# Kernel tuning notes

Hardware: AMD Instinct MI355X
Metric: run time of the kernel (lower is better)

The kernel has to match this reference:

```python
import jax, jax.numpy as jnp
import numpy as np
import math


def _get_slopes(n):
    def pow2(n):
        start = 2 ** (-2 ** (-(math.log2(n) - 3)))
        return [start * start ** i for i in range(n)]
    if math.log2(n).is_integer():
        return pow2(n)
    c = 2 ** math.floor(math.log2(n))
    return pow2(c) + _get_slopes(2 * c)[0::2][: n - c]


NUM_HEADS = 16


def setup_inputs() -> dict:
    slopes = jnp.asarray(np.array(_get_slopes(NUM_HEADS), dtype=np.float32))
    return {"slopes": slopes, "seq_len": 2048, "batch_size": 4}


def reference(slopes, seq_len, batch_size):
    # relative position |i - j|: (S, S)
    pos = jnp.arange(seq_len)
    rel = jnp.abs(pos[:, None] - pos[None, :]).astype(slopes.dtype)
    # (H, S, S): -slope_h * |i - j|
    bias = -slopes[:, None, None] * rel[None, :, :]
    # torch .repeat(batch_size, 1, 1) -> (B*H, S, S)
    return jnp.tile(bias, (batch_size, 1, 1))
```

## Files before the change

### kernel.cpp

```cpp
#include <hip/hip_runtime.h>

#define NUM_HEADS 16u

__global__ __launch_bounds__(256) void alibi_bias_kernel(
    const float* __restrict__ slopes,
    const int* __restrict__ seq_p,
    float* __restrict__ out,
    unsigned int n_total)
{
    const unsigned int S  = (unsigned int)seq_p[0];
    const unsigned int S4 = S >> 2;
    const unsigned int n4 = n_total >> 2;
    const unsigned int stride = gridDim.x * blockDim.x;
    float4* __restrict__ out4 = (float4*)out;

    for (unsigned int v = blockIdx.x * blockDim.x + threadIdx.x; v < n4; v += stride) {
        unsigned int jv  = v % S4;
        unsigned int row = v / S4;
        unsigned int i   = row % S;
        unsigned int h   = (row / S) % NUM_HEADS;

        float nslope = -slopes[h];
        int   ii = (int)i;
        int   j0 = (int)(jv << 2);

        float4 o;
        o.x = nslope * (float)abs(ii - j0);
        o.y = nslope * (float)abs(ii - (j0 + 1));
        o.z = nslope * (float)abs(ii - (j0 + 2));
        o.w = nslope * (float)abs(ii - (j0 + 3));
        out4[v] = o;
    }

    for (unsigned int e = (n4 << 2) + blockIdx.x * blockDim.x + threadIdx.x;
         e < n_total; e += stride) {
        unsigned int j   = e % S;
        unsigned int row = e / S;
        unsigned int i   = row % S;
        unsigned int h   = (row / S) % NUM_HEADS;
        out[e] = -slopes[h] * (float)abs((int)i - (int)j);
    }
}

extern "C" void kernel_launch(void* const* d_in, const int* in_sizes, int n_in,
                              void* d_out, int out_size, void* d_ws, size_t ws_size,
                              hipStream_t stream) {
    const float* slopes = (const float*)d_in[0];
    const int*   seq_p  = (const int*)d_in[1];
    float*       out    = (float*)d_out;

    unsigned int n  = (unsigned int)out_size;
    unsigned int n4 = n >> 2;

    const int block = 256;
    unsigned int blocks_needed = (n4 + block - 1) / block;
    unsigned int grid = blocks_needed < 2048u ? blocks_needed : 2048u;
    if (grid < 1u) grid = 1u;

    alibi_bias_kernel<<<dim3(grid), dim3(block), 0, stream>>>(slopes, seq_p, out, n);
}
```

Measured before the change: 203.9 us.

## Process row-aligned chunks per block with nontemporal vector stores

Each block now handles whole 2048-element chunks that lie inside a single row, so the row, head and slope are worked out once per chunk rather than per float4 with divisions. Each thread writes two float4s using nontemporal stores, which avoids polluting the cache on this write-only output. The grid grows to up to 16384 blocks. The fast path needs S to be a multiple of 2048; any other length falls back to a scalar loop.

```diff
diff --git a/kernel.cpp b/kernel.cpp
--- a/kernel.cpp
+++ b/kernel.cpp
@@ -1,6 +1,9 @@
 #include <hip/hip_runtime.h>
 
 #define NUM_HEADS 16u
+#define CHUNK 2048u
+
+typedef float f32x4 __attribute__((ext_vector_type(4)));
 
 __global__ __launch_bounds__(256) void alibi_bias_kernel(
     const float* __restrict__ slopes,
@@ -8,31 +11,42 @@
     float* __restrict__ out,
     unsigned int n_total)
 {
-    const unsigned int S  = (unsigned int)seq_p[0];
-    const unsigned int S4 = S >> 2;
-    const unsigned int n4 = n_total >> 2;
-    const unsigned int stride = gridDim.x * blockDim.x;
-    float4* __restrict__ out4 = (float4*)out;
+    const unsigned int S = (unsigned int)seq_p[0];
 
-    for (unsigned int v = blockIdx.x * blockDim.x + threadIdx.x; v < n4; v += stride) {
-        unsigned int jv  = v % S4;
-        unsigned int row = v / S4;
-        unsigned int i   = row % S;
-        unsigned int h   = (row / S) % NUM_HEADS;
+    if ((S % CHUNK) == 0u) {
+        const unsigned int nchunks = n_total / CHUNK;
+        for (unsigned int c = blockIdx.x; c < nchunks; c += gridDim.x) {
+            const unsigned int base = c * CHUNK;
+            const unsigned int row  = base / S;
+            const unsigned int jst  = base - row * S;
+            const unsigned int i    = row % S;
+            const unsigned int h    = (row / S) % NUM_HEADS;
+            const float nslope = -slopes[h];
 
-        float nslope = -slopes[h];
-        int   ii = (int)i;
-        int   j0 = (int)(jv << 2);
+            const int j0 = (int)(jst + (threadIdx.x << 2));
+            float d0 = (float)((int)i - j0);
+            f32x4* __restrict__ o4 =
+                (f32x4*)(out + base) + threadIdx.x;
 
-        float4 o;
-        o.x = nslope * (float)abs(ii - j0);
-        o.y = nslope * (float)abs(ii - (j0 + 1));
-        o.z = nslope * (float)abs(ii - (j0 + 2));
-        o.w = nslope * (float)abs(ii - (j0 + 3));
-        out4[v] = o;
+            f32x4 o;
+            o.x = nslope * fabsf(d0);
+            o.y = nslope * fabsf(d0 - 1.0f);
+            o.z = nslope * fabsf(d0 - 2.0f);
+            o.w = nslope * fabsf(d0 - 3.0f);
+            __builtin_nontemporal_store(o, o4);
+
+            const float d1 = d0 - 1024.0f;
+            o.x = nslope * fabsf(d1);
+            o.y = nslope * fabsf(d1 - 1.0f);
+            o.z = nslope * fabsf(d1 - 2.0f);
+            o.w = nslope * fabsf(d1 - 3.0f);
+            __builtin_nontemporal_store(o, o4 + 256);
+        }
+        return;
     }
 
-    for (unsigned int e = (n4 << 2) + blockIdx.x * blockDim.x + threadIdx.x;
+    const unsigned int stride = gridDim.x * blockDim.x;
+    for (unsigned int e = blockIdx.x * blockDim.x + threadIdx.x;
          e < n_total; e += stride) {
         unsigned int j   = e % S;
         unsigned int row = e / S;
@@ -49,12 +63,11 @@
     const int*   seq_p  = (const int*)d_in[1];
     float*       out    = (float*)d_out;
 
-    unsigned int n  = (unsigned int)out_size;
-    unsigned int n4 = n >> 2;
+    const unsigned int n = (unsigned int)out_size;
 
     const int block = 256;
-    unsigned int blocks_needed = (n4 + block - 1) / block;
-    unsigned int grid = blocks_needed < 2048u ? blocks_needed : 2048u;
+    unsigned int nchunks = (n + CHUNK - 1) / CHUNK;
+    unsigned int grid = nchunks < 16384u ? nchunks : 16384u;
     if (grid < 1u) grid = 1u;
 
     alibi_bias_kernel<<<dim3(grid), dim3(block), 0, stream>>>(slopes, seq_p, out, n);
```

New measurement: 201.1 us. No clear change (-1.4%).
